# Kernel optimization log

Measured on AMD Instinct MI355X. Metric: run time of the kernel, lower is better.

Reference implementation:

```python
import jax, jax.numpy as jnp
import numpy as np

EPS_WSUM = 1e-12
EPS_NORM = 1e-12


def setup_inputs() -> dict:
    key = jax.random.key(0)
    ks = jax.random.split(key, 8)
    N, E, D = 100000, 800000, 128
    x = jax.random.normal(ks[0], (N, D), dtype=jnp.float32)
    edge_index = jax.random.randint(ks[1], (2, E), 0, N, dtype=jnp.int64)
    edge_weight = jax.random.uniform(ks[2], (E,), dtype=jnp.float32)
    # Linear(in_dim*2, out_dim): weight [out, 2*in], bias [out]
    W1 = jax.random.normal(ks[3], (D, 2 * D), dtype=jnp.float32) * (1.0 / np.sqrt(2 * D))
    b1 = jnp.zeros((D,), dtype=jnp.float32)
    W2 = jax.random.normal(ks[4], (D, 2 * D), dtype=jnp.float32) * (1.0 / np.sqrt(2 * D))
    b2 = jnp.zeros((D,), dtype=jnp.float32)
    return {"x": x, "edge_index": edge_index, "edge_weight": edge_weight,
            "W1": W1, "b1": b1, "W2": W2, "b2": b2}


def _weighted_neighbor_mean(x, src, dst, w):
    # messages: gather neighbor features at dst, weight per-edge  [E, D]
    msgs = x[dst] * w[:, None]
    num_nodes = x.shape[0]
    agg = jax.ops.segment_sum(msgs, src, num_segments=num_nodes)   # [N, D]
    wsum = jax.ops.segment_sum(w, src, num_segments=num_nodes)     # [N]
    return agg / jnp.maximum(wsum, EPS_WSUM)[:, None]


def _sage_layer(x, src, dst, w, W, b):
    neigh = _weighted_neighbor_mean(x, src, dst, w)
    h = jnp.concatenate([x, neigh], axis=1)          # [N, 2D]
    h = h @ W.T + b                                   # [N, D]
    return jax.nn.relu(h)


def reference(x, edge_index, edge_weight, W1, b1, W2, b2):
    src = edge_index[0]
    dst = edge_index[1]
    h = _sage_layer(x, src, dst, edge_weight, W1, b1)
    h = _sage_layer(h, src, dst, edge_weight, W2, b2)
    # F.normalize(dim=1): x / max(||x||_2, eps)
    norm = jnp.linalg.norm(h, axis=1, keepdims=True)
    return h / jnp.maximum(norm, EPS_NORM)
```

## Files before the change

### kernel.cpp

```cpp
#include <hip/hip_runtime.h>
#include <hip/hip_bf16.h>

#define D 128
#define BSH 8
#define BMASK 255
#define CSTRIDE 32

typedef __attribute__((ext_vector_type(8))) short bf16x8;
typedef __attribute__((ext_vector_type(4))) float f32x4;
typedef unsigned short u16;
typedef unsigned int u32;

__device__ inline u16 f2bf(float f) {
    union { float f; u32 u; } v; v.f = f;
    u32 r = v.u + 0x7FFFu + ((v.u >> 16) & 1u);
    return (u16)(r >> 16);
}

__global__ void cast3_kernel(const float* __restrict__ a, const float* __restrict__ b,
                             const float* __restrict__ c, u16* __restrict__ oa,
                             u16* __restrict__ ob, u16* __restrict__ oc,
                             int na4, int nw4,
                             int* __restrict__ bCursor, int nbuk, int cap) {
    int i = blockIdx.x * blockDim.x + threadIdx.x;
    if (i < nbuk) bCursor[i * CSTRIDE] = i * cap;
    const float* in; u16* out; int k;
    if (i < na4)                { in = a; out = oa; k = i; }
    else if (i < na4 + nw4)     { in = b; out = ob; k = i - na4; }
    else if (i < na4 + 2 * nw4) { in = c; out = oc; k = i - na4 - nw4; }
    else return;
    float4 v = *(const float4*)(in + (size_t)k * 4);
    u32 lo = (u32)f2bf(v.x) | ((u32)f2bf(v.y) << 16);
    u32 hi = (u32)f2bf(v.z) | ((u32)f2bf(v.w) << 16);
    *(uint2*)(out + (size_t)k * 4) = make_uint2(lo, hi);
}

__global__ void partition_kernel(const int* __restrict__ src, const int* __restrict__ dst,
                                 const float* __restrict__ w, int* __restrict__ bucketCursor,
                                 uint2* __restrict__ temp, int E, int nbuk) {
    __shared__ int cnt[1024];
    __shared__ int base[1024];
    int per = (E + gridDim.x - 1) / gridDim.x;
    int lo = blockIdx.x * per;
    int hi = min(E, lo + per);
    for (int i = threadIdx.x; i < nbuk; i += blockDim.x) cnt[i] = 0;
    __syncthreads();
    for (int i = lo + threadIdx.x; i < hi; i += blockDim.x)
        atomicAdd(&cnt[src[i] >> BSH], 1);
    __syncthreads();
    for (int i = threadIdx.x; i < nbuk; i += blockDim.x)
        base[i] = cnt[i] ? atomicAdd(&bucketCursor[i * CSTRIDE], cnt[i]) : 0;
    __syncthreads();
    for (int i = threadIdx.x; i < nbuk; i += blockDim.x) cnt[i] = 0;
    __syncthreads();
    for (int i = lo + threadIdx.x; i < hi; i += blockDim.x) {
        int s = src[i];
        int b = s >> BSH;
        int off = atomicAdd(&cnt[b], 1);
        temp[base[b] + off] =
            make_uint2((u32)dst[i] | ((u32)(s & BMASK) << 17), __float_as_uint(w[i]));
    }
}

__global__ void bucket_csr(const uint2* __restrict__ temp, const int* __restrict__ bucketEnd,
                           uint2* __restrict__ rowse, uint2* __restrict__ edge,
                           int N, int cap) {
    int b = blockIdx.x;
    int lo = b * cap;
    int hi = bucketEnd[b * CSTRIDE];
    int t = threadIdx.x;
    __shared__ int deg_l[256];
    __shared__ int sc[256];
    __shared__ int cur[256];
    deg_l[t] = 0;
    __syncthreads();
    for (int i = lo + t; i < hi; i += 256)
        atomicAdd(&deg_l[temp[i].x >> 17], 1);
    __syncthreads();
    int mydeg = deg_l[t];
    sc[t] = mydeg;
    __syncthreads();
    for (int off = 1; off < 256; off <<= 1) {
        int v = (t >= off) ? sc[t - off] : 0;
        __syncthreads();
        sc[t] += v;
        __syncthreads();
    }
    int excl = (t == 0) ? 0 : sc[t - 1];
    int gnode = (b << BSH) + t;
    if (gnode < N) rowse[gnode] = make_uint2((u32)(lo + excl), (u32)mydeg);
    cur[t] = excl;
    __syncthreads();
    for (int i = lo + t; i < hi; i += 256) {
        uint2 r = temp[i];
        int p = atomicAdd(&cur[r.x >> 17], 1);
        edge[lo + p] = make_uint2(r.x & 0x1FFFFu, r.y);
    }
}

__global__ void aggregate_kernel(const u16* __restrict__ feat,
                                 const uint2* __restrict__ rowse,
                                 const uint2* __restrict__ edge,
                                 u16* __restrict__ neigh, int n) {
    const char* fb = (const char*)feat;
    int wv   = blockIdx.x * 4 + (threadIdx.x >> 6);
    int lane = threadIdx.x & 63;
    int grp  = lane >> 4;
    int l16  = lane & 15;
    int node0 = wv * 4;
    if (node0 >= n) return;

    int begs[4], degs[4];
#pragma unroll
    for (int i = 0; i < 4; ++i) {
        int nd = node0 + i; if (nd > n - 1) nd = n - 1;
        uint2 se = rowse[nd];
        begs[i] = __builtin_amdgcn_readfirstlane((int)se.x);
        degs[i] = __builtin_amdgcn_readfirstlane((int)se.y);
    }

#pragma unroll 1
    for (int i = 0; i < 4; ++i) {
        int node = node0 + i;
        if (node >= n) break;
        int beg = begs[i];
        int end = beg + degs[i];
        float acc[8] = {0.f, 0.f, 0.f, 0.f, 0.f, 0.f, 0.f, 0.f};
        float ws = 0.f;
        for (int j = beg; j < end; j += 8) {
            int ia = j + grp;
            int ib = j + 4 + grp;
            int ca = ia < end ? ia : end - 1;
            int cb = ib < end ? ib : end - 1;
            uint2 ea = edge[ca];
            uint2 eb = edge[cb];
            float wa = (ia < end) ? __uint_as_float(ea.y) : 0.f;
            float wb = (ib < end) ? __uint_as_float(eb.y) : 0.f;
            uint4 ua = *(const uint4*)(fb + (size_t)ea.x * 256u + (u32)l16 * 16u);
            uint4 ub = *(const uint4*)(fb + (size_t)eb.x * 256u + (u32)l16 * 16u);
            u32 va[4] = {ua.x, ua.y, ua.z, ua.w};
            u32 vb[4] = {ub.x, ub.y, ub.z, ub.w};
#pragma unroll
            for (int kk = 0; kk < 4; ++kk) {
                acc[kk * 2]     += __uint_as_float(va[kk] << 16) * wa
                                 + __uint_as_float(vb[kk] << 16) * wb;
                acc[kk * 2 + 1] += __uint_as_float(va[kk] & 0xFFFF0000u) * wa
                                 + __uint_as_float(vb[kk] & 0xFFFF0000u) * wb;
            }
            ws += wa + wb;
        }
#pragma unroll
        for (int kk = 0; kk < 8; ++kk) {
            acc[kk] += __shfl_xor(acc[kk], 16);
            acc[kk] += __shfl_xor(acc[kk], 32);
        }
        ws += __shfl_xor(ws, 16);
        ws += __shfl_xor(ws, 32);
        float inv = 1.0f / fmaxf(ws, 1e-12f);
        if (grp == 0) {
            u32 o0 = (u32)f2bf(acc[0] * inv) | ((u32)f2bf(acc[1] * inv) << 16);
            u32 o1 = (u32)f2bf(acc[2] * inv) | ((u32)f2bf(acc[3] * inv) << 16);
            u32 o2 = (u32)f2bf(acc[4] * inv) | ((u32)f2bf(acc[5] * inv) << 16);
            u32 o3 = (u32)f2bf(acc[6] * inv) | ((u32)f2bf(acc[7] * inv) << 16);
            *(uint4*)(neigh + (size_t)node * D + l16 * 8) = make_uint4(o0, o1, o2, o3);
        }
    }
}

template <bool NORM>
__global__ void __launch_bounds__(512, 2)
sage_gemm(const u16* __restrict__ axb,
          const u16* __restrict__ aneigh,
          const u16* __restrict__ Wb,
          const float* __restrict__ bias,
          u16* __restrict__ outB,
          float* __restrict__ outF,
          int n) {
    __shared__ __attribute__((aligned(16))) char smem[65536];

    const int tid  = threadIdx.x;
    const int wave = tid >> 6;
    const int lane = tid & 63;
    const int quad = lane >> 4;
    const int l16  = lane & 15;
    const int r0   = blockIdx.x * 256 + wave * 32;

    bf16x8 a[2][8];
    {
        int ra = r0 + l16;        if (ra >= n) ra = n - 1;
        int rb = r0 + 16 + l16;   if (rb >= n) rb = n - 1;
        const u16* p00 = axb    + (size_t)ra * D + quad * 8;
        const u16* p10 = axb    + (size_t)rb * D + quad * 8;
        const u16* p01 = aneigh + (size_t)ra * D + quad * 8;
        const u16* p11 = aneigh + (size_t)rb * D + quad * 8;
#pragma unroll
        for (int kk = 0; kk < 4; ++kk) {
            a[0][kk] = *(const bf16x8*)(p00 + kk * 32);
            a[1][kk] = *(const bf16x8*)(p10 + kk * 32);
        }
#pragma unroll
        for (int kk = 0; kk < 4; ++kk) {
            a[0][4 + kk] = *(const bf16x8*)(p01 + kk * 32);
            a[1][4 + kk] = *(const bf16x8*)(p11 + kk * 32);
        }
    }

#pragma unroll
    for (int it = 0; it < 8; ++it) {
        int e = it * 512 + tid;
        int c  = e >> 5;
        int kc = e & 31;
        uint4 v = *(const uint4*)(Wb + (size_t)c * 256 + kc * 8);
        u32 off = (((u32)c << 9) + ((u32)kc << 4)) ^ (((u32)c & 7u) << 4);
        *(uint4*)(smem + off) = v;
    }
    __syncthreads();

    f32x4 acc[2][8];
#pragma unroll
    for (int s = 0; s < 2; ++s)
#pragma unroll
        for (int c = 0; c < 8; ++c)
            acc[s][c] = (f32x4){0.f, 0.f, 0.f, 0.f};

#pragma unroll
    for (int kk = 0; kk < 8; ++kk) {
#pragma unroll
        for (int c = 0; c < 8; ++c) {
            u32 col = (u32)(c * 16 + l16);
            u32 off = ((col << 9) + ((u32)(kk * 4 + quad) << 4)) ^ ((col & 7u) << 4);
            bf16x8 b = *(const bf16x8*)(smem + off);
            acc[0][c] = __builtin_amdgcn_mfma_f32_16x16x32_bf16(a[0][kk], b, acc[0][c], 0, 0, 0);
            acc[1][c] = __builtin_amdgcn_mfma_f32_16x16x32_bf16(a[1][kk], b, acc[1][c], 0, 0, 0);
        }
    }

    __syncthreads();

    float bvals[8];
#pragma unroll
    for (int c = 0; c < 8; ++c) bvals[c] = bias[c * 16 + l16];

    if (NORM) {
        float* stg = (float*)smem + wave * 2048;
#pragma unroll
        for (int s = 0; s < 2; ++s) {
#pragma unroll
            for (int reg = 0; reg < 4; ++reg) {
                float v[8];
#pragma unroll
                for (int c = 0; c < 8; ++c)
                    v[c] = fmaxf(acc[s][c][reg] + bvals[c], 0.0f);
                float ss = 0.f;
#pragma unroll
                for (int c = 0; c < 8; ++c) ss += v[c] * v[c];
                ss += __shfl_xor(ss, 1);
                ss += __shfl_xor(ss, 2);
                ss += __shfl_xor(ss, 4);
                ss += __shfl_xor(ss, 8);
                float inv = 1.0f / fmaxf(sqrtf(ss), 1e-12f);
#pragma unroll
                for (int c = 0; c < 8; ++c)
                    stg[(quad * 4 + reg) * 128 + c * 16 + l16] = v[c] * inv;
            }
#pragma unroll
            for (int p = 0; p < 8; ++p) {
                int lr = 2 * p + (lane >> 5);
                int grow = r0 + s * 16 + lr;
                float4 val = *(float4*)&stg[lr * 128 + (lane & 31) * 4];
                if (grow < n)
                    *(float4*)(outF + (size_t)grow * D + (lane & 31) * 4) = val;
            }
        }
    } else {
        u16* stg = (u16*)smem + wave * 2048;
#pragma unroll
        for (int s = 0; s < 2; ++s) {
#pragma unroll
            for (int reg = 0; reg < 4; ++reg) {
#pragma unroll
                for (int c = 0; c < 8; ++c) {
                    float v = fmaxf(acc[s][c][reg] + bvals[c], 0.0f);
                    stg[(quad * 4 + reg) * 128 + c * 16 + l16] = f2bf(v);
                }
            }
#pragma unroll
            for (int p = 0; p < 4; ++p) {
                int lr = 4 * p + (lane >> 4);
                int grow = r0 + s * 16 + lr;
                uint4 val = *(uint4*)&stg[lr * 128 + l16 * 8];
                if (grow < n)
                    *(uint4*)(outB + (size_t)grow * D + l16 * 8) = val;
            }
        }
    }
}

extern "C" void kernel_launch(void* const* d_in, const int* in_sizes, int n_in,
                              void* d_out, int out_size, void* d_ws, size_t ws_size,
                              hipStream_t stream) {
    const float* x  = (const float*)d_in[0];
    const int*   ei = (const int*)d_in[1];
    const float* ew = (const float*)d_in[2];
    const float* W1 = (const float*)d_in[3];
    const float* b1 = (const float*)d_in[4];
    const float* W2 = (const float*)d_in[5];
    const float* b2 = (const float*)d_in[6];
    float* out = (float*)d_out;

    const int E = in_sizes[2];
    const int N = in_sizes[0] / D;
    const int nbuk = (N + BMASK) >> BSH;
    const int CAP = ((2 * (E / nbuk + 1) + 1023) / 1024) * 1024;

    const int* src = ei;
    const int* dst = ei + E;

    char* p = (char*)d_ws;
    auto alloc = [&](size_t bytes) { char* r = p; p += (bytes + 255) & ~(size_t)255; return r; };
    u16*   xb      = (u16*)  alloc((size_t)N * D * sizeof(u16));
    u16*   hB      = (u16*)  alloc((size_t)N * D * sizeof(u16));
    u16*   neighB  = (u16*)  alloc((size_t)N * D * sizeof(u16));
    uint2* temp    = (uint2*)alloc(((size_t)nbuk * CAP + 64) * 8);
    uint2* edge    = (uint2*)alloc(((size_t)nbuk * CAP + 64) * 8);
    u16*   Wb1     = (u16*)  alloc((size_t)D * 2 * D * sizeof(u16));
    u16*   Wb2     = (u16*)  alloc((size_t)D * 2 * D * sizeof(u16));
    uint2* rowse   = (uint2*)alloc((size_t)N * sizeof(uint2));
    int*   bCursor = (int*)  alloc((size_t)(nbuk * CSTRIDE + 64) * sizeof(int));

    const int gemmGrid = (N + 255) / 256;
    const int n4 = N * D / 4;
    const int w4 = D * 2 * D / 4;
    const int castTotal = n4 + 2 * w4;
    const int aggGrid = (N + 15) / 16;

    cast3_kernel    <<<(castTotal + 255) / 256, 256, 0, stream>>>(x, W1, W2, xb, Wb1, Wb2,
                                                                  n4, w4, bCursor, nbuk, CAP);
    partition_kernel<<<256, 256, 0, stream>>>(src, dst, ew, bCursor, temp, E, nbuk);
    bucket_csr      <<<nbuk, 256, 0, stream>>>(temp, bCursor, rowse, edge, N, CAP);

    aggregate_kernel<<<aggGrid, 256, 0, stream>>>(xb, rowse, edge, neighB, N);
    sage_gemm<false><<<gemmGrid, 512, 0, stream>>>(xb, neighB, Wb1, b1, hB, nullptr, N);

    aggregate_kernel<<<aggGrid, 256, 0, stream>>>(hB, rowse, edge, neighB, N);
    sage_gemm<true><<<gemmGrid, 512, 0, stream>>>(hB, neighB, Wb2, b2, nullptr, out, N);
}
```

Measured before the change: 259.0 us.

## Fuse neighbor aggregation into the SAGE GEMM kernel via shared memory

Replaces the separate aggregate and GEMM kernels with one fused kernel per layer. Each 512-thread block aggregates 128 nodes into shared memory as bf16 and then runs the MFMA GEMM against the two halves of W, loaded into LDS one after the other. This removes the write and re-read of the neighbor buffer in global memory and two kernel launches. The gather loop is also unrolled to 16 edges per iteration. In exchange, aggregation now shares a block with GEMM work, 64KB of static LDS is allocated per block while launch bounds request 4 blocks, and per-block load imbalance from varying node degrees may stall the GEMM phase.

Result: slower. 289.7 us (+11.8%).

```diff
diff --git a/kernel.cpp b/kernel.cpp
--- a/kernel.cpp
+++ b/kernel.cpp
@@ -98,140 +98,152 @@
     }
 }
 
-__global__ void aggregate_kernel(const u16* __restrict__ feat,
-                                 const uint2* __restrict__ rowse,
-                                 const uint2* __restrict__ edge,
-                                 u16* __restrict__ neigh, int n) {
+template <bool NORM>
+__global__ void __launch_bounds__(512, 4)
+sage_fused(const u16* __restrict__ feat,
+           const uint2* __restrict__ rowse,
+           const uint2* __restrict__ edge,
+           const u16* __restrict__ Wb,
+           const float* __restrict__ bias,
+           u16* __restrict__ outB,
+           float* __restrict__ outF,
+           int n) {
+    __shared__ __attribute__((aligned(16))) char smem[65536];
     const char* fb = (const char*)feat;
-    int wv   = blockIdx.x * 4 + (threadIdx.x >> 6);
-    int lane = threadIdx.x & 63;
-    int grp  = lane >> 4;
-    int l16  = lane & 15;
-    int node0 = wv * 4;
-    if (node0 >= n) return;
-
-    int begs[4], degs[4];
-#pragma unroll
-    for (int i = 0; i < 4; ++i) {
-        int nd = node0 + i; if (nd > n - 1) nd = n - 1;
-        uint2 se = rowse[nd];
-        begs[i] = __builtin_amdgcn_readfirstlane((int)se.x);
-        degs[i] = __builtin_amdgcn_readfirstlane((int)se.y);
-    }
-
-#pragma unroll 1
-    for (int i = 0; i < 4; ++i) {
-        int node = node0 + i;
-        if (node >= n) break;
-        int beg = begs[i];
-        int end = beg + degs[i];
-        float acc[8] = {0.f, 0.f, 0.f, 0.f, 0.f, 0.f, 0.f, 0.f};
-        float ws = 0.f;
-        for (int j = beg; j < end; j += 8) {
-            int ia = j + grp;
-            int ib = j + 4 + grp;
-            int ca = ia < end ? ia : end - 1;
-            int cb = ib < end ? ib : end - 1;
-            uint2 ea = edge[ca];
-            uint2 eb = edge[cb];
-            float wa = (ia < end) ? __uint_as_float(ea.y) : 0.f;
-            float wb = (ib < end) ? __uint_as_float(eb.y) : 0.f;
-            uint4 ua = *(const uint4*)(fb + (size_t)ea.x * 256u + (u32)l16 * 16u);
-            uint4 ub = *(const uint4*)(fb + (size_t)eb.x * 256u + (u32)l16 * 16u);
-            u32 va[4] = {ua.x, ua.y, ua.z, ua.w};
-            u32 vb[4] = {ub.x, ub.y, ub.z, ub.w};
-#pragma unroll
-            for (int kk = 0; kk < 4; ++kk) {
-                acc[kk * 2]     += __uint_as_float(va[kk] << 16) * wa
-                                 + __uint_as_float(vb[kk] << 16) * wb;
-                acc[kk * 2 + 1] += __uint_as_float(va[kk] & 0xFFFF0000u) * wa
-                                 + __uint_as_float(vb[kk] & 0xFFFF0000u) * wb;
-            }
-            ws += wa + wb;
-        }
-#pragma unroll
-        for (int kk = 0; kk < 8; ++kk) {
-            acc[kk] += __shfl_xor(acc[kk], 16);
-            acc[kk] += __shfl_xor(acc[kk], 32);
-        }
-        ws += __shfl_xor(ws, 16);
-        ws += __shfl_xor(ws, 32);
-        float inv = 1.0f / fmaxf(ws, 1e-12f);
-        if (grp == 0) {
-            u32 o0 = (u32)f2bf(acc[0] * inv) | ((u32)f2bf(acc[1] * inv) << 16);
-            u32 o1 = (u32)f2bf(acc[2] * inv) | ((u32)f2bf(acc[3] * inv) << 16);
-            u32 o2 = (u32)f2bf(acc[4] * inv) | ((u32)f2bf(acc[5] * inv) << 16);
-            u32 o3 = (u32)f2bf(acc[6] * inv) | ((u32)f2bf(acc[7] * inv) << 16);
-            *(uint4*)(neigh + (size_t)node * D + l16 * 8) = make_uint4(o0, o1, o2, o3);
-        }
-    }
-}
-
-template <bool NORM>
-__global__ void __launch_bounds__(512, 2)
-sage_gemm(const u16* __restrict__ axb,
-          const u16* __restrict__ aneigh,
-          const u16* __restrict__ Wb,
-          const float* __restrict__ bias,
-          u16* __restrict__ outB,
-          float* __restrict__ outF,
-          int n) {
-    __shared__ __attribute__((aligned(16))) char smem[65536];
 
     const int tid  = threadIdx.x;
     const int wave = tid >> 6;
     const int lane = tid & 63;
+    const int grp  = lane >> 4;
+    const int l16  = lane & 15;
+    const int r0   = blockIdx.x * 128;
+
+#pragma unroll
+    for (int it = 0; it < 4; ++it) {
+        int e  = it * 512 + tid;
+        int c2 = e >> 4;
+        int kc = e & 15;
+        uint4 v = *(const uint4*)(Wb + (size_t)c2 * 256 + kc * 8);
+        *(uint4*)(smem + 32768 + c2 * 256 + ((u32)(kc ^ (c2 & 15)) << 4)) = v;
+    }
+
+    {
+        int ndl = r0 + wave * 16 + l16;
+        if (ndl > n - 1) ndl = n - 1;
+        uint2 seL = rowse[ndl];
+#pragma unroll 1
+        for (int i = 0; i < 16; ++i) {
+            int beg = __builtin_amdgcn_readfirstlane(__shfl((int)seL.x, i));
+            int deg = __builtin_amdgcn_readfirstlane(__shfl((int)seL.y, i));
+            int end = beg + deg;
+            float acc[8] = {0.f, 0.f, 0.f, 0.f, 0.f, 0.f, 0.f, 0.f};
+            float ws = 0.f;
+            for (int j = beg; j < end; j += 16) {
+                int i0 = j + grp, i1 = j + 4 + grp, i2 = j + 8 + grp, i3 = j + 12 + grp;
+                int c0 = i0 < end ? i0 : end - 1;
+                int c1 = i1 < end ? i1 : end - 1;
+                int c2 = i2 < end ? i2 : end - 1;
+                int c3 = i3 < end ? i3 : end - 1;
+                uint2 e0 = edge[c0], e1 = edge[c1], e2 = edge[c2], e3 = edge[c3];
+                float w0 = (i0 < end) ? __uint_as_float(e0.y) : 0.f;
+                float w1 = (i1 < end) ? __uint_as_float(e1.y) : 0.f;
+                float w2 = (i2 < end) ? __uint_as_float(e2.y) : 0.f;
+                float w3 = (i3 < end) ? __uint_as_float(e3.y) : 0.f;
+                uint4 u0 = *(const uint4*)(fb + (size_t)e0.x * 256u + (u32)l16 * 16u);
+                uint4 u1 = *(const uint4*)(fb + (size_t)e1.x * 256u + (u32)l16 * 16u);
+                uint4 u2 = *(const uint4*)(fb + (size_t)e2.x * 256u + (u32)l16 * 16u);
+                uint4 u3 = *(const uint4*)(fb + (size_t)e3.x * 256u + (u32)l16 * 16u);
+                u32 a0[4] = {u0.x, u0.y, u0.z, u0.w};
+                u32 a1[4] = {u1.x, u1.y, u1.z, u1.w};
+                u32 a2[4] = {u2.x, u2.y, u2.z, u2.w};
+                u32 a3[4] = {u3.x, u3.y, u3.z, u3.w};
+#pragma unroll
+                for (int kk = 0; kk < 4; ++kk) {
+                    acc[kk * 2]     += __uint_as_float(a0[kk] << 16) * w0
+                                     + __uint_as_float(a1[kk] << 16) * w1
+                                     + __uint_as_float(a2[kk] << 16) * w2
+                                     + __uint_as_float(a3[kk] << 16) * w3;
+                    acc[kk * 2 + 1] += __uint_as_float(a0[kk] & 0xFFFF0000u) * w0
+                                     + __uint_as_float(a1[kk] & 0xFFFF0000u) * w1
+                                     + __uint_as_float(a2[kk] & 0xFFFF0000u) * w2
+                                     + __uint_as_float(a3[kk] & 0xFFFF0000u) * w3;
+                }
+                ws += w0 + w1 + w2 + w3;
+            }
+#pragma unroll
+            for (int kk = 0; kk < 8; ++kk) {
+                acc[kk] += __shfl_xor(acc[kk], 16);
+                acc[kk] += __shfl_xor(acc[kk], 32);
+            }
+            ws += __shfl_xor(ws, 16);
+            ws += __shfl_xor(ws, 32);
+            float inv = 1.0f / fmaxf(ws, 1e-12f);
+            if (grp == 0) {
+                u32 o0 = (u32)f2bf(acc[0] * inv) | ((u32)f2bf(acc[1] * inv) << 16);
+                u32 o1 = (u32)f2bf(acc[2] * inv) | ((u32)f2bf(acc[3] * inv) << 16);
+                u32 o2 = (u32)f2bf(acc[4] * inv) | ((u32)f2bf(acc[5] * inv) << 16);
+                u32 o3 = (u32)f2bf(acc[6] * inv) | ((u32)f2bf(acc[7] * inv) << 16);
+                int lr = wave * 16 + i;
+                *(uint4*)(smem + lr * 256 + ((u32)(l16 ^ (lr & 15)) << 4)) =
+                    make_uint4(o0, o1, o2, o3);
+            }
+        }
+    }
+
+    bf16x8 ax[4];
+    {
+        int ra = r0 + wave * 16 + l16;
+        if (ra >= n) ra = n - 1;
+        const u16* pax = feat + (size_t)ra * D + (lane >> 4) * 8;
+#pragma unroll
+        for (int kk = 0; kk < 4; ++kk)
+            ax[kk] = *(const bf16x8*)(pax + kk * 32);
+    }
+    uint4 breg[4];
+#pragma unroll
+    for (int it = 0; it < 4; ++it) {
+        int e  = it * 512 + tid;
+        int c2 = e >> 4;
+        int kc = e & 15;
+        breg[it] = *(const uint4*)(Wb + (size_t)c2 * 256 + 128 + kc * 8);
+    }
+
+    __syncthreads();
+
     const int quad = lane >> 4;
-    const int l16  = lane & 15;
-    const int r0   = blockIdx.x * 256 + wave * 32;
-
-    bf16x8 a[2][8];
-    {
-        int ra = r0 + l16;        if (ra >= n) ra = n - 1;
-        int rb = r0 + 16 + l16;   if (rb >= n) rb = n - 1;
-        const u16* p00 = axb    + (size_t)ra * D + quad * 8;
-        const u16* p10 = axb    + (size_t)rb * D + quad * 8;
-        const u16* p01 = aneigh + (size_t)ra * D + quad * 8;
-        const u16* p11 = aneigh + (size_t)rb * D + quad * 8;
-#pragma unroll
-        for (int kk = 0; kk < 4; ++kk) {
-            a[0][kk] = *(const bf16x8*)(p00 + kk * 32);
-            a[1][kk] = *(const bf16x8*)(p10 + kk * 32);
-        }
-#pragma unroll
-        for (int kk = 0; kk < 4; ++kk) {
-            a[0][4 + kk] = *(const bf16x8*)(p01 + kk * 32);
-            a[1][4 + kk] = *(const bf16x8*)(p11 + kk * 32);
-        }
-    }
-
-#pragma unroll
-    for (int it = 0; it < 8; ++it) {
-        int e = it * 512 + tid;
-        int c  = e >> 5;
-        int kc = e & 31;
-        uint4 v = *(const uint4*)(Wb + (size_t)c * 256 + kc * 8);
-        u32 off = (((u32)c << 9) + ((u32)kc << 4)) ^ (((u32)c & 7u) << 4);
-        *(uint4*)(smem + off) = v;
-    }
-    __syncthreads();
-
-    f32x4 acc[2][8];
-#pragma unroll
-    for (int s = 0; s < 2; ++s)
-#pragma unroll
-        for (int c = 0; c < 8; ++c)
-            acc[s][c] = (f32x4){0.f, 0.f, 0.f, 0.f};
-
-#pragma unroll
-    for (int kk = 0; kk < 8; ++kk) {
+    f32x4 acc[8];
+#pragma unroll
+    for (int c = 0; c < 8; ++c) acc[c] = (f32x4){0.f, 0.f, 0.f, 0.f};
+
+#pragma unroll
+    for (int kk = 0; kk < 4; ++kk) {
+        u32 slot = ((u32)(kk * 4 + quad) ^ (u32)l16) << 4;
 #pragma unroll
         for (int c = 0; c < 8; ++c) {
-            u32 col = (u32)(c * 16 + l16);
-            u32 off = ((col << 9) + ((u32)(kk * 4 + quad) << 4)) ^ ((col & 7u) << 4);
-            bf16x8 b = *(const bf16x8*)(smem + off);
-            acc[0][c] = __builtin_amdgcn_mfma_f32_16x16x32_bf16(a[0][kk], b, acc[0][c], 0, 0, 0);
-            acc[1][c] = __builtin_amdgcn_mfma_f32_16x16x32_bf16(a[1][kk], b, acc[1][c], 0, 0, 0);
+            bf16x8 b = *(const bf16x8*)(smem + 32768 + (c * 16 + l16) * 256 + slot);
+            acc[c] = __builtin_amdgcn_mfma_f32_16x16x32_bf16(ax[kk], b, acc[c], 0, 0, 0);
+        }
+    }
+
+    __syncthreads();
+
+#pragma unroll
+    for (int it = 0; it < 4; ++it) {
+        int e  = it * 512 + tid;
+        int c2 = e >> 4;
+        int kc = e & 15;
+        *(uint4*)(smem + 32768 + c2 * 256 + ((u32)(kc ^ (c2 & 15)) << 4)) = breg[it];
+    }
+    __syncthreads();
+
+#pragma unroll
+    for (int kk = 0; kk < 4; ++kk) {
+        u32 slot = ((u32)(kk * 4 + quad) ^ (u32)l16) << 4;
+        bf16x8 an = *(const bf16x8*)(smem + (wave * 16 + l16) * 256 + slot);
+#pragma unroll
+        for (int c = 0; c < 8; ++c) {
+            bf16x8 b = *(const bf16x8*)(smem + 32768 + (c * 16 + l16) * 256 + slot);
+            acc[c] = __builtin_amdgcn_mfma_f32_16x16x32_bf16(an, b, acc[c], 0, 0, 0);
         }
     }
 
@@ -244,54 +256,48 @@
     if (NORM) {
         float* stg = (float*)smem + wave * 2048;
 #pragma unroll
-        for (int s = 0; s < 2; ++s) {
-#pragma unroll
-            for (int reg = 0; reg < 4; ++reg) {
-                float v[8];
-#pragma unroll
-                for (int c = 0; c < 8; ++c)
-                    v[c] = fmaxf(acc[s][c][reg] + bvals[c], 0.0f);
-                float ss = 0.f;
-#pragma unroll
-                for (int c = 0; c < 8; ++c) ss += v[c] * v[c];
-                ss += __shfl_xor(ss, 1);
-                ss += __shfl_xor(ss, 2);
-                ss += __shfl_xor(ss, 4);
-                ss += __shfl_xor(ss, 8);
-                float inv = 1.0f / fmaxf(sqrtf(ss), 1e-12f);
-#pragma unroll
-                for (int c = 0; c < 8; ++c)
-                    stg[(quad * 4 + reg) * 128 + c * 16 + l16] = v[c] * inv;
-            }
-#pragma unroll
-            for (int p = 0; p < 8; ++p) {
-                int lr = 2 * p + (lane >> 5);
-                int grow = r0 + s * 16 + lr;
-                float4 val = *(float4*)&stg[lr * 128 + (lane & 31) * 4];
-                if (grow < n)
-                    *(float4*)(outF + (size_t)grow * D + (lane & 31) * 4) = val;
-            }
+        for (int reg = 0; reg < 4; ++reg) {
+            float v[8];
+#pragma unroll
+            for (int c = 0; c < 8; ++c)
+                v[c] = fmaxf(acc[c][reg] + bvals[c], 0.0f);
+            float ss = 0.f;
+#pragma unroll
+            for (int c = 0; c < 8; ++c) ss += v[c] * v[c];
+            ss += __shfl_xor(ss, 1);
+            ss += __shfl_xor(ss, 2);
+            ss += __shfl_xor(ss, 4);
+            ss += __shfl_xor(ss, 8);
+            float inv = 1.0f / fmaxf(sqrtf(ss), 1e-12f);
+#pragma unroll
+            for (int c = 0; c < 8; ++c)
+                stg[(quad * 4 + reg) * 128 + c * 16 + l16] = v[c] * inv;
+        }
+#pragma unroll
+        for (int p = 0; p < 8; ++p) {
+            int lr = 2 * p + (lane >> 5);
+            int grow = r0 + wave * 16 + lr;
+            float4 val = *(float4*)&stg[lr * 128 + (lane & 31) * 4];
+            if (grow < n)
+                *(float4*)(outF + (size_t)grow * D + (lane & 31) * 4) = val;
         }
     } else {
         u16* stg = (u16*)smem + wave * 2048;
 #pragma unroll
-        for (int s = 0; s < 2; ++s) {
-#pragma unroll
-            for (int reg = 0; reg < 4; ++reg) {
-#pragma unroll
-                for (int c = 0; c < 8; ++c) {
-                    float v = fmaxf(acc[s][c][reg] + bvals[c], 0.0f);
-                    stg[(quad * 4 + reg) * 128 + c * 16 + l16] = f2bf(v);
-                }
+        for (int reg = 0; reg < 4; ++reg) {
+#pragma unroll
+            for (int c = 0; c < 8; ++c) {
+                float v = fmaxf(acc[c][reg] + bvals[c], 0.0f);
+                stg[(quad * 4 + reg) * 128 + c * 16 + l16] = f2bf(v);
             }
-#pragma unroll
-            for (int p = 0; p < 4; ++p) {
-                int lr = 4 * p + (lane >> 4);
-                int grow = r0 + s * 16 + lr;
-                uint4 val = *(uint4*)&stg[lr * 128 + l16 * 8];
-                if (grow < n)
-                    *(uint4*)(outB + (size_t)grow * D + l16 * 8) = val;
-            }
+        }
+#pragma unroll
+        for (int p = 0; p < 4; ++p) {
+            int lr = 4 * p + (lane >> 4);
+            int grow = r0 + wave * 16 + lr;
+            uint4 val = *(uint4*)&stg[lr * 128 + l16 * 8];
+            if (grow < n)
+                *(uint4*)(outB + (size_t)grow * D + l16 * 8) = val;
         }
     }
 }
@@ -320,7 +326,6 @@
     auto alloc = [&](size_t bytes) { char* r = p; p += (bytes + 255) & ~(size_t)255; return r; };
     u16*   xb      = (u16*)  alloc((size_t)N * D * sizeof(u16));
     u16*   hB      = (u16*)  alloc((size_t)N * D * sizeof(u16));
-    u16*   neighB  = (u16*)  alloc((size_t)N * D * sizeof(u16));
     uint2* temp    = (uint2*)alloc(((size_t)nbuk * CAP + 64) * 8);
     uint2* edge    = (uint2*)alloc(((size_t)nbuk * CAP + 64) * 8);
     u16*   Wb1     = (u16*)  alloc((size_t)D * 2 * D * sizeof(u16));
@@ -328,20 +333,18 @@
     uint2* rowse   = (uint2*)alloc((size_t)N * sizeof(uint2));
     int*   bCursor = (int*)  alloc((size_t)(nbuk * CSTRIDE + 64) * sizeof(int));
 
-    const int gemmGrid = (N + 255) / 256;
+    const int fusedGrid = (N + 127) / 128;
     const int n4 = N * D / 4;
     const int w4 = D * 2 * D / 4;
     const int castTotal = n4 + 2 * w4;
-    const int aggGrid = (N + 15) / 16;
 
     cast3_kernel    <<<(castTotal + 255) / 256, 256, 0, stream>>>(x, W1, W2, xb, Wb1, Wb2,
                                                                   n4, w4, bCursor, nbuk, CAP);
     partition_kernel<<<256, 256, 0, stream>>>(src, dst, ew, bCursor, temp, E, nbuk);
     bucket_csr      <<<nbuk, 256, 0, stream>>>(temp, bCursor, rowse, edge, N, CAP);
 
-    aggregate_kernel<<<aggGrid, 256, 0, stream>>>(xb, rowse, edge, neighB, N);
-    sage_gemm<false><<<gemmGrid, 512, 0, stream>>>(xb, neighB, Wb1, b1, hB, nullptr, N);
-
-    aggregate_kernel<<<aggGrid, 256, 0, stream>>>(hB, rowse, edge, neighB, N);
-    sage_gemm<true><<<gemmGrid, 512, 0, stream>>>(hB, neighB, Wb2, b2, nullptr, out, N);
-}
+    sage_fused<false><<<fusedGrid, 512, 0, stream>>>(xb, rowse, edge, Wb1, b1,
+                                                     hB, nullptr, N);
+    sage_fused<true><<<fusedGrid, 512, 0, stream>>>(hB, rowse, edge, Wb2, b2,
+                                                    nullptr, out, N);
+}
```
